# Optimization experiments

Hardware: AMD Instinct MI355X
Metric: run time of the kernel (lower is better)

## Reference

```python
import jax, jax.numpy as jnp
import numpy as np

S, B, N, L, ND = 16, 64, 10000, 128, 1  # seq_len, batch, nodes, latent_dim, node_dim


def setup_inputs() -> dict:
    key = jax.random.key(0)
    ks = jax.random.split(key, 20)
    D_msg = ND + L        # GRU input: [node_feat || time_enc]
    D_h = ND + 2 * L      # attention input: [x || memory || time_enc]
    g = lambda k, shp, s: (jax.random.normal(k, shp, jnp.float32) * s)
    return {
        "x": jax.random.normal(ks[0], (S, B, N, ND), jnp.float32),
        "t": jax.random.uniform(ks[1], (S, B, N, 1), jnp.float32),
        "source": jax.random.randint(ks[2], (S, B, 1), 0, N),
        "target": jax.random.randint(ks[3], (S, B, 1), 0, N),
        "neighbor_mask": jax.random.randint(ks[4], (S, B, N), 0, 2).astype(jnp.bool_),
        # TimeEncoder: cos(t @ w + b)
        "time_w": g(ks[5], (1, L), 1.0),
        "time_b": g(ks[6], (L,), 1.0),
        # MemoryUpdater: GRUCell(input=D_msg, hidden=L)
        "W_ih": g(ks[7], (3 * L, D_msg), 1.0 / np.sqrt(D_msg)),
        "W_hh": g(ks[8], (3 * L, L), 1.0 / np.sqrt(L)),
        "b_ih": jnp.zeros((3 * L,), jnp.float32),
        "b_hh": jnp.zeros((3 * L,), jnp.float32),
        # Attention projections (D_h -> L)
        "Wq": g(ks[9], (D_h, L), 1.0 / np.sqrt(D_h)),
        "bq": jnp.zeros((L,), jnp.float32),
        "Wk": g(ks[10], (D_h, L), 1.0 / np.sqrt(D_h)),
        "bk": jnp.zeros((L,), jnp.float32),
        "Wv": g(ks[11], (D_h, L), 1.0 / np.sqrt(D_h)),
        "bv": jnp.zeros((L,), jnp.float32),
        # final Linear(L -> 1)
        "W_out": g(ks[12], (L, 1), 1.0 / np.sqrt(L)),
        "b_out": jnp.zeros((1,), jnp.float32),
    }


def reference(x, t, source, target, neighbor_mask, time_w, time_b,
              W_ih, W_hh, b_ih, b_hh, Wq, bq, Wk, bk, Wv, bv, W_out, b_out):
    s_len, bsz, n_nodes, _ = x.shape
    lat = time_w.shape[1]
    scale = 1.0 / jnp.sqrt(jnp.float32(lat))
    bidx = jnp.arange(bsz)

    def time_enc(tt):  # [..., 1] -> [..., L]
        return jnp.cos(tt @ time_w + time_b)

    def gru(msg, h):  # torch GRUCell semantics
        gi = msg @ W_ih.T + b_ih
        gh = h @ W_hh.T + b_hh
        i_r, i_z, i_n = jnp.split(gi, 3, axis=-1)
        h_r, h_z, h_n = jnp.split(gh, 3, axis=-1)
        r = jax.nn.sigmoid(i_r + h_r)
        z = jax.nn.sigmoid(i_z + h_z)
        n = jnp.tanh(i_n + r * h_n)
        return (1.0 - z) * n + z * h

    def step(memory, batch):
        xb, tb, src, tgt, mask = batch
        src = src[:, 0]
        tgt = tgt[:, 0]
        dt = time_enc(tb)  # [B, N, L]
        # 1. update memory at source and target nodes
        msg_s = jnp.concatenate([xb[bidx, src], dt[bidx, src]], axis=-1)  # [B, ND+L]
        msg_t = jnp.concatenate([xb[bidx, tgt], dt[bidx, tgt]], axis=-1)
        new_s = gru(msg_s, memory[src])
        new_t = gru(msg_t, memory[tgt])
        mem = memory.at[src].set(new_s).at[tgt].set(new_t)
        # 2. embedding: target query
        tvec = jnp.concatenate([xb[bidx, tgt], mem[tgt]], axis=-1)  # [B, ND+L]
        enc0 = jnp.broadcast_to(jnp.cos(time_b), (bsz, lat))  # time_enc(t=0)
        target_h = jnp.concatenate([tvec, enc0], axis=-1)  # [B, ND+2L]
        # per-node keys/values
        h = jnp.concatenate(
            [xb, jnp.broadcast_to(mem, (bsz, n_nodes, lat)), dt], axis=-1)  # [B, N, ND+2L]
        q = target_h @ Wq + bq          # [B, L]
        k = h @ Wk + bk                 # [B, N, L]
        v = h @ Wv + bv                 # [B, N, L]
        scores = jnp.einsum("bl,bnl->bn", q, k) * scale
        scores = jnp.where(mask, scores, jnp.float32(-1e9))
        attn = jax.nn.softmax(scores, axis=-1)
        z = jnp.einsum("bn,bnl->bl", attn, v)
        logit = z @ W_out + b_out       # [B, 1]
        return mem, logit

    mem0 = jnp.zeros((n_nodes, lat), jnp.float32)
    _, logits = jax.lax.scan(step, mem0, (x, t, source, target, neighbor_mask))
    return logits  # [S, B, 1]
```

## Files before the change

### kernel.cpp

```cpp
#include <hip/hip_runtime.h>
#include <math.h>

#define S_LEN 16
#define BSZ   64
#define NN    10000
#define LAT   128
#define DH    257
#define KTAB  1024
#define CSTRIDE (KTAB + 8)
#define FSTRIDE (KTAB + 4)
#define NTILE 64
#define NTILES 157
#define STEP_BLKS 350
#define SCALE 0.08838834764831845f
#define NEG1E9 -1000000000.0f

struct KP {
    const float *x, *t;
    const int *source, *target;
    const void *maskp;
    const float *tw, *tb_;
    const float *W_ih, *W_hh, *b_ih, *b_hh;
    const float *Wq, *bq, *Wk, *bk, *Wv, *bv, *W_out, *b_out;
    float *out;
    float *mem;
    float *newh[2], *uT[2], *u0qbk[2], *ftab[2], *partials[2];
    float *gtab, *costab;
    float *wv_out, *vconst, *W_ihT, *W_hhT, *BT, *uc, *kw0, *abk, *scal;
    int *modep;
};

__device__ void gru_a_block(const KP& p, float* sm, int r, int snext, int sprev, int zeroH) {
    int tid = threadIdx.x;
    int par = snext & 1;
    float* msg = sm;
    float* h   = sm + 132;
    float* gi3 = sm + 260;
    float* gh3 = sm + 644;
    float* hn  = sm + 1028;
    int*   itab = (int*)(sm + 1156);
    float* axv = sm + 1284;
    unsigned long long* amask = (unsigned long long*)(sm + 1288);
    float* udt = sm + 1296;
    float* red2 = sm + 1424;
    float* fpart = sm + 1440;

    int b = r & 63;
    int idx = (r < 64) ? p.source[snext * BSZ + b] : p.target[snext * BSZ + b];
    if (sprev >= 0 && tid < 128)
        itab[tid] = (tid < 64) ? p.source[sprev * BSZ + tid] : p.target[sprev * BSZ + (tid - 64)];
    const float* xs = p.x + (size_t)(snext * BSZ + b) * NN;
    const float* ts = p.t + (size_t)(snext * BSZ + b) * NN;
    if (tid == 0) msg[0] = xs[idx];
    if (tid < 128) {
        float tv = ts[idx];
        msg[1 + tid] = __cosf(tv * p.tw[tid] + p.tb_[tid]);
    }
    __syncthreads();
    int w = -1;
    if (sprev >= 0) {
        for (int k = 127; k >= 0; --k) if (itab[k] == idx) { w = k; break; }
    }
    if (tid < 128) {
        h[tid] = zeroH ? 0.f
               : (w >= 0 ? p.newh[par ^ 1][w * LAT + tid] : p.mem[(size_t)idx * LAT + tid]);
    }
    __syncthreads();
    if (tid < 128) {
        int j = tid;
        float a0 = p.b_ih[j], a1 = p.b_ih[128 + j], a2 = p.b_ih[256 + j];
#pragma unroll 4
        for (int d = 0; d < 129; ++d) {
            float m = msg[d];
            const float* col = p.W_ihT + d * 384;
            a0 += m * col[j]; a1 += m * col[128 + j]; a2 += m * col[256 + j];
        }
        gi3[j] = a0; gi3[128 + j] = a1; gi3[256 + j] = a2;
    } else {
        int j = tid - 128;
        float a0 = p.b_hh[j], a1 = p.b_hh[128 + j], a2 = p.b_hh[256 + j];
#pragma unroll 4
        for (int l = 0; l < 128; ++l) {
            float hv = h[l];
            const float* col = p.W_hhT + l * 384;
            a0 += hv * col[j]; a1 += hv * col[128 + j]; a2 += hv * col[256 + j];
        }
        gh3[j] = a0; gh3[128 + j] = a1; gh3[256 + j] = a2;
    }
    __syncthreads();
    if (tid < 128) {
        int j = tid;
        float rr = 1.f / (1.f + __expf(-(gi3[j] + gh3[j])));
        float zz = 1.f / (1.f + __expf(-(gi3[128 + j] + gh3[128 + j])));
        float nn2 = tanhf(gi3[256 + j] + rr * gh3[256 + j]);
        float val = (1.f - zz) * nn2 + zz * h[j];
        hn[j] = val;
        p.newh[par][r * LAT + j] = val;
    }
    if (r < 64) return;

    int rT = r - 64;
    int* tg = itab;
    __syncthreads();
    if (tid < 64) tg[tid] = p.target[snext * BSZ + tid];
    __syncthreads();
    unsigned long long mask = 0;
    if (tid < 64) {
        int myt = tg[tid]; int sl = 0;
        for (int k = 0; k < 64; ++k) if (tg[k] == myt) sl = k;
        mask = __ballot(sl == rT);
    }
    if (tid == 0) *amask = mask;
    __syncthreads();
    unsigned long long bl = *amask;
    float* u0qb = p.u0qbk[par];
    float* uTb  = p.uT[par];
    float* ftb  = p.ftab[par];
    while (bl) {
        int b2 = __ffsll((long long)bl) - 1; bl &= bl - 1;
        if (tid == 0) *axv = p.x[(size_t)(snext * BSZ + b2) * NN + tg[b2]];
        __syncthreads();
        float xv = *axv;
        {
            int d = tid;
            float a0 = 0.f, a1 = 0.f;
#pragma unroll 4
            for (int l = 0; l < 128; l += 2) {
                a0 += hn[l] * p.BT[l * 260 + d];
                a1 += hn[l + 1] * p.BT[(l + 1) * 260 + d];
            }
            float a = p.uc[d] + xv * p.kw0[d] + a0 + a1;
            if (d == 0) u0qb[b2] = a;
            else if (d <= 128) uTb[(d - 1) * BSZ + b2] = a;
            else udt[d - 129] = a;
            if (tid == 0) {
                float c0 = 0.f, c1 = 0.f;
#pragma unroll 4
                for (int l = 0; l < 128; l += 2) {
                    c0 += hn[l] * p.BT[l * 260 + 256];
                    c1 += hn[l + 1] * p.BT[(l + 1) * 260 + 256];
                }
                udt[127] = p.uc[256] + xv * p.kw0[256] + c0 + c1;
            }
        }
        if (tid >= 192) {
            int i = tid - 192;
            float a = hn[i] * p.abk[i] + hn[64 + i] * p.abk[64 + i];
            for (int off = 32; off; off >>= 1) a += __shfl_down(a, off, 64);
            if (i == 0) u0qb[64 + b2] = p.scal[0] + xv * p.scal[1] + a;
        }
        __syncthreads();
        {
            int pi = tid & 127, lc = tid >> 7;
            int l0 = lc * 64;
            float a0x = 0.f, a0y = 0.f, a0z = 0.f, a0w = 0.f;
            float a1x = 0.f, a1y = 0.f, a1z = 0.f, a1w = 0.f;
#pragma unroll 4
            for (int l = l0; l < l0 + 64; ++l) {
                float ul = udt[l];
                const float* cp = &p.costab[l * CSTRIDE + pi * 8];
                float4 c0 = *(const float4*)cp;
                float4 c1 = *(const float4*)(cp + 4);
                a0x += ul * c0.x; a0y += ul * c0.y; a0z += ul * c0.z; a0w += ul * c0.w;
                a1x += ul * c1.x; a1y += ul * c1.y; a1z += ul * c1.z; a1w += ul * c1.w;
            }
            if (lc) {
                float* fp = &fpart[pi * 8];
                *(float4*)fp = make_float4(a0x, a0y, a0z, a0w);
                *(float4*)(fp + 4) = make_float4(a1x, a1y, a1z, a1w);
            }
            if (pi == 127) {
                float a = 0.f;
                for (int l = l0; l < l0 + 64; ++l) a += udt[l] * p.costab[l * CSTRIDE + KTAB];
                red2[lc] = a;
            }
            __syncthreads();
            if (lc == 0) {
                const float* fp = &fpart[pi * 8];
                a0x += fp[0]; a0y += fp[1]; a0z += fp[2]; a0w += fp[3];
                a1x += fp[4]; a1y += fp[5]; a1z += fp[6]; a1w += fp[7];
                float* fo = &ftb[b2 * FSTRIDE + pi * 8];
                *(float4*)fo = make_float4(a0x, a0y, a0z, a0w);
                *(float4*)(fo + 4) = make_float4(a1x, a1y, a1z, a1w);
            }
            if (tid == 0) ftb[b2 * FSTRIDE + KTAB] = red2[0] + red2[1];
        }
        __syncthreads();
    }
}

__device__ void combine256(const float* __restrict__ partials, const float* __restrict__ vconst,
                           float* __restrict__ out, float* sm, int b, int ps) {
    int tid = threadIdx.x;
    float m = -3.0e38f, d = 0.f, n = 0.f;
    if (tid < NTILES) {
        float4 v = *((const float4*)partials + b * NTILES + tid);
        m = v.x; d = v.y; n = v.z;
    }
#pragma unroll
    for (int off = 32; off; off >>= 1) {
        float mo = __shfl_down(m, off, 64);
        float d2 = __shfl_down(d, off, 64);
        float n2 = __shfl_down(n, off, 64);
        float M = fmaxf(m, mo);
        float e1 = __expf(m - M), e2 = __expf(mo - M);
        d = d * e1 + d2 * e2; n = n * e1 + n2 * e2; m = M;
    }
    float* red = sm;
    int w = tid >> 6;
    if ((tid & 63) == 0) { red[w * 3] = m; red[w * 3 + 1] = d; red[w * 3 + 2] = n; }
    __syncthreads();
    if (tid == 0) {
        float M = red[0], D = red[1], Nm = red[2];
        for (int k2 = 1; k2 < 4; ++k2) {
            float m2 = red[k2 * 3], d2 = red[k2 * 3 + 1], n2 = red[k2 * 3 + 2];
            float M2 = fmaxf(M, m2);
            float e1 = __expf(M - M2), e2 = __expf(m2 - M2);
            D = D * e1 + d2 * e2; Nm = Nm * e1 + n2 * e2; M = M2;
        }
        out[ps * BSZ + b] = Nm / D + vconst[0];
    }
}

__global__ __launch_bounds__(256) void setup_kernel(KP p) {
    int blk = blockIdx.x, tid = threadIdx.x;
    __shared__ float sm[256];
    if (blk < 256) {
        int gtid = blk * 256 + tid;
        const int GS = 256 * 256;
        for (int i = gtid; i < 129 * 384; i += GS) { int d = i / 384, j = i % 384; p.W_ihT[i] = p.W_ih[j * 129 + d]; }
        for (int i = gtid; i < 128 * 384; i += GS) { int l = i / 384, j = i % 384; p.W_hhT[i] = p.W_hh[j * 128 + l]; }
        for (int pp = gtid; pp <= KTAB; pp += GS) {
            float tv = (float)pp * (1.0f / KTAB);
            for (int l = 0; l < 128; ++l) p.costab[l * CSTRIDE + pp] = __cosf(tv * p.tw[l] + p.tb_[l]);
        }
    } else if (blk == 256) {
        for (int d = tid; d < DH; d += 256) {
            float a = 0.f;
            for (int j = 0; j < LAT; ++j) a += p.Wv[d * LAT + j] * p.W_out[j];
            p.wv_out[d] = a;
        }
        if (tid == 0) {
            float a = p.b_out[0];
            for (int j = 0; j < LAT; ++j) a += p.bv[j] * p.W_out[j];
            p.vconst[0] = a;
        }
        __shared__ int hasHigh, hasFloat;
        if (tid == 0) { hasHigh = 0; hasFloat = 0; }
        __syncthreads();
        const int* mask = (const int*)p.maskp;
        for (int i = tid; i < 4096; i += 256) {
            int v = mask[i];
            if ((unsigned)v > 1u) atomicOr(&hasHigh, 1);
            if (v == 0x3F800000) atomicOr(&hasFloat, 1);
        }
        __syncthreads();
        if (tid == 0) p.modep[0] = hasFloat ? 2 : (hasHigh ? 1 : 0);
    } else if (blk < 385) {
        int l = blk - 257;
        float* vrow = sm;
        if (tid < 128) vrow[tid] = p.Wq[(1 + l) * LAT + tid];
        __syncthreads();
        for (int d = tid; d < DH; d += 256) {
            const float* wkr = p.Wk + d * LAT;
            float a = 0.f;
#pragma unroll 4
            for (int j = 0; j < 128; ++j) a += wkr[j] * vrow[j];
            p.BT[l * 260 + d] = a;
        }
    } else if (blk == 385) {
        float* vrow = sm;
        if (tid < 128) vrow[tid] = p.Wq[tid];
        __syncthreads();
        for (int d = tid; d < DH; d += 256) {
            const float* wkr = p.Wk + d * LAT;
            float a = 0.f;
#pragma unroll 4
            for (int j = 0; j < 128; ++j) a += wkr[j] * vrow[j];
            p.kw0[d] = a;
        }
    } else if (blk == 386) {
        __shared__ float cosv[128], qc[128];
        if (tid < 128) cosv[tid] = __cosf(p.tb_[tid]);
        __syncthreads();
        if (tid < 128) {
            float a = p.bq[tid];
            for (int j = 0; j < 128; ++j) a += cosv[j] * p.Wq[(129 + j) * LAT + tid];
            qc[tid] = a;
        }
        __syncthreads();
        for (int d = tid; d < DH; d += 256) {
            const float* wkr = p.Wk + d * LAT;
            float a = 0.f;
#pragma unroll 4
            for (int j = 0; j < 128; ++j) a += wkr[j] * qc[j];
            p.uc[d] = a;
        }
    } else {
        __shared__ float bkv[128], cosv[128], tpart[128];
        if (tid < 128) { bkv[tid] = p.bk[tid]; cosv[tid] = __cosf(p.tb_[tid]); }
        __syncthreads();
        if (tid < 128) {
            const float* wqr = p.Wq + (1 + tid) * LAT;
            float a = 0.f;
#pragma unroll 4
            for (int j = 0; j < 128; ++j) a += wqr[j] * bkv[j];
            p.abk[tid] = a;
        } else {
            int j = tid - 128;
            const float* wqr = p.Wq + (129 + j) * LAT;
            float a = 0.f;
#pragma unroll 4
            for (int l = 0; l < 128; ++l) a += wqr[l] * bkv[l];
            tpart[j] = cosv[j] * a;
        }
        __syncthreads();
        if (tid == 0) {
            float s0 = 0.f, s1 = 0.f;
            for (int l = 0; l < 128; ++l) { s0 += p.bq[l] * bkv[l]; s1 += p.Wq[l] * bkv[l]; }
            for (int j = 0; j < 128; ++j) s0 += tpart[j];
            p.scal[0] = s0; p.scal[1] = s1;
        }
    }
}

__global__ __launch_bounds__(256) void pre2_kernel(KP p) {
    __shared__ __align__(16) float sm[2464];
    int blk = blockIdx.x, tid = threadIdx.x;
    if (blk < 5) {
        __shared__ float wv_s[LAT];
        if (tid < LAT) wv_s[tid] = p.wv_out[129 + tid];
        __syncthreads();
        int pp = blk * 256 + tid;
        if (pp <= KTAB) {
            float a = 0.f;
            for (int l = 0; l < 128; ++l) a += wv_s[l] * p.costab[l * CSTRIDE + pp];
            p.gtab[pp] = a;
        }
        return;
    }
    gru_a_block(p, sm, blk - 5, 0, -1, 1);
}

__global__ __launch_bounds__(256) void step_kernel(KP p, int s) {
    __shared__ __align__(16) float sm[9472];
    int blk = blockIdx.x, tid = threadIdx.x;
    int par = s & 1;

    if (blk >= 157 && blk < 285) {
        if (s < S_LEN - 1)
            gru_a_block(p, sm, blk - 157, s + 1, s, 0);
        return;
    }
    if (blk == 285) {
        int* idxs  = (int*)sm;
        int* alive = idxs + 128;
        if (tid < 128) idxs[tid] = (tid < 64) ? p.source[s * BSZ + tid] : p.target[s * BSZ + (tid - 64)];
        __syncthreads();
        if (tid < 128) {
            int i2 = idxs[tid];
            int a = 1;
            for (int r2 = tid + 1; r2 < 128; ++r2)
                if (idxs[r2] == i2) { a = 0; break; }
            alive[tid] = a;
        }
        __syncthreads();
        int row = tid >> 1, q2 = tid & 1;
        if (alive[row]) {
            const float4* srcp = (const float4*)(p.newh[par] + row * LAT + q2 * 64);
            float4* dstp = (float4*)(p.mem + (size_t)idxs[row] * LAT + q2 * 64);
#pragma unroll
            for (int j = 0; j < 16; ++j) dstp[j] = srcp[j];
        }
        return;
    }
    if (blk >= 286) {
        if (s > 0) combine256(p.partials[par ^ 1], p.vconst, p.out, sm, blk - 286, s - 1);
        return;
    }

    float* memT   = sm;
    float* uTs    = sm + 4608;
    float* memv_s = sm + 8960;
    float* wv_s   = sm + 9024;
    float* u0_s   = sm + 9152;
    float* qbk_s  = sm + 9216;
    int*   idxs   = (int*)(sm + 9280);
    int*   prow   = idxs + 128;
    int tile = blk;
    int n0 = tile * NTILE;
    int tb = tid >> 4, tn = tid & 15;
    int nvalid = NN - n0; if (nvalid > NTILE) nvalid = NTILE;

    if (tid < 128) wv_s[tid] = p.wv_out[1 + tid];
    if (tid < 64) {
        u0_s[tid] = p.u0qbk[par][tid];
        qbk_s[tid] = p.u0qbk[par][64 + tid];
        memv_s[tid] = 0.f;
    }
    if (tid < 128) idxs[tid] = (tid < 64) ? p.source[s * BSZ + tid] : p.target[s * BSZ + (tid - 64)];
    __syncthreads();
    if (tid < 64) {
        int node = n0 + tid; int w = -1;
        for (int k = 127; k >= 0; --k) if (idxs[k] == node) { w = k; break; }
        prow[tid] = w;
    }

    float acc[4][4];
#pragma unroll
    for (int i = 0; i < 4; ++i)
#pragma unroll
        for (int j = 0; j < 4; ++j) acc[i][j] = 0.f;

    const float* nh = p.newh[par];
    for (int l0 = 0; l0 < 128; l0 += 64) {
        __syncthreads();
        {
            int n_l = tid & 63, lq = (tid >> 6) * 16;
            if (n_l < nvalid) {
                int w = prow[n_l];
                const float* mrow = (w >= 0) ? (nh + w * LAT + l0 + lq)
                                             : (p.mem + (size_t)(n0 + n_l) * LAT + l0 + lq);
                float4 a0 = *(const float4*)(mrow + 0);
                float4 a1 = *(const float4*)(mrow + 4);
                float4 a2 = *(const float4*)(mrow + 8);
                float4 a3 = *(const float4*)(mrow + 12);
                memT[(lq + 0) * 72 + n_l] = a0.x; memT[(lq + 1) * 72 + n_l] = a0.y;
                memT[(lq + 2) * 72 + n_l] = a0.z; memT[(lq + 3) * 72 + n_l] = a0.w;
                memT[(lq + 4) * 72 + n_l] = a1.x; memT[(lq + 5) * 72 + n_l] = a1.y;
                memT[(lq + 6) * 72 + n_l] = a1.z; memT[(lq + 7) * 72 + n_l] = a1.w;
                memT[(lq + 8) * 72 + n_l] = a2.x; memT[(lq + 9) * 72 + n_l] = a2.y;
                memT[(lq + 10) * 72 + n_l] = a2.z; memT[(lq + 11) * 72 + n_l] = a2.w;
                memT[(lq + 12) * 72 + n_l] = a3.x; memT[(lq + 13) * 72 + n_l] = a3.y;
                memT[(lq + 14) * 72 + n_l] = a3.z; memT[(lq + 15) * 72 + n_l] = a3.w;
            } else {
                for (int j = 0; j < 16; ++j) memT[(lq + j) * 72 + n_l] = 0.f;
            }
        }
        {
            int bq4 = (tid & 15) * 4;
            int ll = (tid >> 4) * 4;
            const float* uTb = p.uT[par];
            for (int j = 0; j < 4; ++j) {
                float4 v = *(const float4*)&uTb[(l0 + ll + j) * BSZ + bq4];
                *(float4*)&uTs[(ll + j) * 68 + bq4] = v;
            }
        }
        __syncthreads();
        if (tid < 64) {
            float a = memv_s[tid];
            for (int l = 0; l < 64; ++l) a += wv_s[l0 + l] * memT[l * 72 + tid];
            memv_s[tid] = a;
        }
        for (int l = 0; l < 64; ++l) {
            float4 uv = *(const float4*)&uTs[l * 68 + tb * 4];
            float4 mv = *(const float4*)&memT[l * 72 + tn * 4];
            acc[0][0] += uv.x * mv.x; acc[0][1] += uv.x * mv.y; acc[0][2] += uv.x * mv.z; acc[0][3] += uv.x * mv.w;
            acc[1][0] += uv.y * mv.x; acc[1][1] += uv.y * mv.y; acc[1][2] += uv.y * mv.z; acc[1][3] += uv.y * mv.w;
            acc[2][0] += uv.z * mv.x; acc[2][1] += uv.z * mv.y; acc[2][2] += uv.z * mv.z; acc[2][3] += uv.z * mv.w;
            acc[3][0] += uv.w * mv.x; acc[3][1] += uv.w * mv.y; acc[3][2] += uv.w * mv.z; acc[3][3] += uv.w * mv.w;
        }
    }
    __syncthreads();

    const float c0 = p.wv_out[0];
    int mode = p.modep[0];
    const int* m32 = (const int*)p.maskp;
    const unsigned char* m8 = (const unsigned char*)p.maskp;
    const float* mf = (const float*)p.maskp;
    const float* gtab = p.gtab;
    const float* ftb = p.ftab[par];

    float pm[4], pd[4], pn[4];
#pragma unroll
    for (int i = 0; i < 4; ++i) { pm[i] = -3.0e38f; pd[i] = 0.f; pn[i] = 0.f; }

    for (int i = 0; i < 4; ++i) {
        int b = tb * 4 + i;
        size_t base = (size_t)(s * BSZ + b) * NN + n0 + tn * 4;
        float xv4[4], tv4[4]; int msk[4], vld[4];
        if (tn * 4 + 3 < nvalid) {
            float4 xx = *(const float4*)(p.x + base);
            float4 tt = *(const float4*)(p.t + base);
            xv4[0] = xx.x; xv4[1] = xx.y; xv4[2] = xx.z; xv4[3] = xx.w;
            tv4[0] = tt.x; tv4[1] = tt.y; tv4[2] = tt.z; tv4[3] = tt.w;
            if (mode == 1) {
                unsigned mw = *(const unsigned*)(m8 + base);
                msk[0] = mw & 0xff; msk[1] = (mw >> 8) & 0xff; msk[2] = (mw >> 16) & 0xff; msk[3] = (mw >> 24) & 0xff;
            } else if (mode == 2) {
                float4 mm = *(const float4*)(mf + base);
                msk[0] = (mm.x != 0.f); msk[1] = (mm.y != 0.f); msk[2] = (mm.z != 0.f); msk[3] = (mm.w != 0.f);
            } else {
                int4 mm = *(const int4*)(m32 + base);
                msk[0] = mm.x; msk[1] = mm.y; msk[2] = mm.z; msk[3] = mm.w;
            }
            vld[0] = vld[1] = vld[2] = vld[3] = 1;
        } else {
            for (int j = 0; j < 4; ++j) {
                int n = tn * 4 + j;
                vld[j] = (n < nvalid);
                if (vld[j]) {
                    xv4[j] = p.x[base + j]; tv4[j] = p.t[base + j];
                    msk[j] = (mode == 1) ? (int)m8[base + j] : (mode == 2) ? (mf[base + j] != 0.f) : m32[base + j];
                } else { xv4[j] = 0.f; tv4[j] = 0.f; msk[j] = 0; }
            }
        }
        const float* ft = ftb + b * FSTRIDE;
#pragma unroll
        for (int j = 0; j < 4; ++j) {
            if (!vld[j]) continue;
            float xv = xv4[j], tv = tv4[j];
            float pq = tv * (float)KTAB;
            pq = fminf(fmaxf(pq, 0.f), (float)KTAB - 0.001f);
            int ii = (int)pq;
            float fr = pq - (float)ii;
            float f0 = ft[ii];
            float fv = f0 + (ft[ii + 1] - f0) * fr;
            float g0 = gtab[ii];
            float gv = g0 + (gtab[ii + 1] - g0) * fr;
            float sc = SCALE * (xv * u0_s[b] + acc[i][j] + fv + qbk_s[b]);
            if (msk[j] == 0) sc = NEG1E9;
            float val = xv * c0 + memv_s[tn * 4 + j] + gv;
            if (sc > pm[i]) {
                float a = __expf(pm[i] - sc);
                pd[i] = pd[i] * a + 1.f;
                pn[i] = pn[i] * a + val;
                pm[i] = sc;
            } else {
                float e = __expf(sc - pm[i]);
                pd[i] += e;
                pn[i] += e * val;
            }
        }
    }
#pragma unroll
    for (int mk2 = 1; mk2 < 16; mk2 <<= 1) {
#pragma unroll
        for (int i = 0; i < 4; ++i) {
            float mo = __shfl_xor(pm[i], mk2);
            float d2 = __shfl_xor(pd[i], mk2);
            float n2 = __shfl_xor(pn[i], mk2);
            float M = fmaxf(pm[i], mo);
            float e1 = __expf(pm[i] - M), e2 = __expf(mo - M);
            pd[i] = pd[i] * e1 + d2 * e2;
            pn[i] = pn[i] * e1 + n2 * e2;
            pm[i] = M;
        }
    }
    if (tn == 0) {
#pragma unroll
        for (int i = 0; i < 4; ++i) {
            int b = tb * 4 + i;
            *(float4*)&p.partials[par][(size_t)(b * NTILES + tile) * 4] = make_float4(pm[i], pd[i], pn[i], 0.f);
        }
    }
}

__global__ __launch_bounds__(256) void tail2_kernel(KP p) {
    __shared__ float sm[16];
    combine256(p.partials[(S_LEN - 1) & 1], p.vconst, p.out, sm, blockIdx.x, S_LEN - 1);
}

extern "C" void kernel_launch(void* const* d_in, const int* in_sizes, int n_in,
                              void* d_out, int out_size, void* d_ws, size_t ws_size,
                              hipStream_t stream) {
    KP kp;
    kp.x      = (const float*)d_in[0];
    kp.t      = (const float*)d_in[1];
    kp.source = (const int*)d_in[2];
    kp.target = (const int*)d_in[3];
    kp.maskp  = (const void*)d_in[4];
    kp.tw     = (const float*)d_in[5];
    kp.tb_    = (const float*)d_in[6];
    kp.W_ih   = (const float*)d_in[7];
    kp.W_hh   = (const float*)d_in[8];
    kp.b_ih   = (const float*)d_in[9];
    kp.b_hh   = (const float*)d_in[10];
    kp.Wq     = (const float*)d_in[11];
    kp.bq     = (const float*)d_in[12];
    kp.Wk     = (const float*)d_in[13];
    kp.bk     = (const float*)d_in[14];
    kp.Wv     = (const float*)d_in[15];
    kp.bv     = (const float*)d_in[16];
    kp.W_out  = (const float*)d_in[17];
    kp.b_out  = (const float*)d_in[18];
    kp.out    = (float*)d_out;

    float* w = (float*)d_ws;
    kp.mem        = w; w += (size_t)NN * LAT;
    kp.newh[0]    = w; w += 128 * LAT;
    kp.newh[1]    = w; w += 128 * LAT;
    kp.uT[0]      = w; w += LAT * BSZ;
    kp.uT[1]      = w; w += LAT * BSZ;
    kp.u0qbk[0]   = w; w += 128;
    kp.u0qbk[1]   = w; w += 128;
    kp.ftab[0]    = w; w += BSZ * FSTRIDE;
    kp.ftab[1]    = w; w += BSZ * FSTRIDE;
    kp.partials[0] = w; w += (size_t)BSZ * NTILES * 4;
    kp.partials[1] = w; w += (size_t)BSZ * NTILES * 4;
    kp.gtab       = w; w += 1056;
    kp.costab     = w; w += LAT * CSTRIDE;
    kp.wv_out     = w; w += 288;
    kp.vconst     = w; w += 32;
    kp.W_ihT      = w; w += 129 * 384;
    kp.W_hhT      = w; w += 128 * 384;
    kp.BT         = w; w += 128 * 260;
    kp.uc         = w; w += 288;
    kp.kw0        = w; w += 288;
    kp.abk        = w; w += 128;
    kp.scal       = w; w += 32;
    kp.modep      = (int*)w; w += 32;

    hipMemsetAsync(kp.mem, 0, (size_t)NN * LAT * sizeof(float), stream);
    setup_kernel<<<388, 256, 0, stream>>>(kp);
    pre2_kernel<<<133, 256, 0, stream>>>(kp);
    for (int s = 0; s < S_LEN; ++s)
        step_kernel<<<STEP_BLKS, 256, 0, stream>>>(kp, s);
    tail2_kernel<<<64, 256, 0, stream>>>(kp);
}
```

Measured before the change: 832.2 us.

## Split attention tiles across batch quarters and prefetch per-node inputs early

Each attention block now handles 16 batch rows of a 64-node tile instead of all 64, so the grid grows from 157 to 628 attention blocks. Each thread keeps one batch row with four accumulators rather than a 4x4 register tile. The x, t and mask loads and the f/g table gathers are issued before the memory-tile GEMM so their latency overlaps it. The price is that every node tile is reloaded and transposed four times, and each block does less arithmetic per load.

```diff
diff --git a/kernel.cpp b/kernel.cpp
--- a/kernel.cpp
+++ b/kernel.cpp
@@ -11,7 +11,12 @@
 #define FSTRIDE (KTAB + 4)
 #define NTILE 64
 #define NTILES 157
-#define STEP_BLKS 350
+#define BSPLIT 4
+#define ATTN_BLKS (NTILES * BSPLIT)
+#define GRU0 ATTN_BLKS
+#define SCAT (ATTN_BLKS + 128)
+#define COMB0 (SCAT + 1)
+#define STEP_BLKS (COMB0 + 64)
 #define SCALE 0.08838834764831845f
 #define NEG1E9 -1000000000.0f
 
@@ -343,16 +348,16 @@
 }
 
 __global__ __launch_bounds__(256) void step_kernel(KP p, int s) {
-    __shared__ __align__(16) float sm[9472];
+    __shared__ __align__(16) float sm[7680];
     int blk = blockIdx.x, tid = threadIdx.x;
     int par = s & 1;
 
-    if (blk >= 157 && blk < 285) {
+    if (blk >= GRU0 && blk < SCAT) {
         if (s < S_LEN - 1)
-            gru_a_block(p, sm, blk - 157, s + 1, s, 0);
+            gru_a_block(p, sm, blk - GRU0, s + 1, s, 0);
         return;
     }
-    if (blk == 285) {
+    if (blk == SCAT) {
         int* idxs  = (int*)sm;
         int* alive = idxs + 128;
         if (tid < 128) idxs[tid] = (tid < 64) ? p.source[s * BSZ + tid] : p.target[s * BSZ + (tid - 64)];
@@ -374,30 +379,82 @@
         }
         return;
     }
-    if (blk >= 286) {
-        if (s > 0) combine256(p.partials[par ^ 1], p.vconst, p.out, sm, blk - 286, s - 1);
+    if (blk >= COMB0) {
+        if (s > 0) combine256(p.partials[par ^ 1], p.vconst, p.out, sm, blk - COMB0, s - 1);
         return;
     }
 
     float* memT   = sm;
     float* uTs    = sm + 4608;
-    float* memv_s = sm + 8960;
-    float* wv_s   = sm + 9024;
-    float* u0_s   = sm + 9152;
-    float* qbk_s  = sm + 9216;
-    int*   idxs   = (int*)(sm + 9280);
-    int*   prow   = idxs + 128;
-    int tile = blk;
-    int n0 = tile * NTILE;
+    float* wv_s   = sm + 7168;
+    float* memv_s = sm + 7296;
+    float* u0_s   = sm + 7360;
+    float* qbk_s  = sm + 7376;
+    int*   idxs   = (int*)(sm + 7392);
+    int*   prow   = (int*)(sm + 7520);
+
+    int tile = blk >> 2, bq = blk & 3;
+    int n0 = tile * NTILE, b0 = bq * 16;
     int tb = tid >> 4, tn = tid & 15;
+    int b = b0 + tb;
     int nvalid = NN - n0; if (nvalid > NTILE) nvalid = NTILE;
 
+    int mode = p.modep[0];
+    const int* m32 = (const int*)p.maskp;
+    const unsigned char* m8 = (const unsigned char*)p.maskp;
+    const float* mf = (const float*)p.maskp;
+    size_t base = (size_t)(s * BSZ + b) * NN + n0 + tn * 4;
+    float xv4[4], tv4[4]; int msk[4], vld[4];
+    if (tn * 4 + 3 < nvalid) {
+        float4 xx = *(const float4*)(p.x + base);
+        float4 tt = *(const float4*)(p.t + base);
+        xv4[0] = xx.x; xv4[1] = xx.y; xv4[2] = xx.z; xv4[3] = xx.w;
+        tv4[0] = tt.x; tv4[1] = tt.y; tv4[2] = tt.z; tv4[3] = tt.w;
+        if (mode == 1) {
+            unsigned mw = *(const unsigned*)(m8 + base);
+            msk[0] = mw & 0xff; msk[1] = (mw >> 8) & 0xff; msk[2] = (mw >> 16) & 0xff; msk[3] = (mw >> 24) & 0xff;
+        } else if (mode == 2) {
+            float4 mm = *(const float4*)(mf + base);
+            msk[0] = (mm.x != 0.f); msk[1] = (mm.y != 0.f); msk[2] = (mm.z != 0.f); msk[3] = (mm.w != 0.f);
+        } else {
+            int4 mm = *(const int4*)(m32 + base);
+            msk[0] = mm.x; msk[1] = mm.y; msk[2] = mm.z; msk[3] = mm.w;
+        }
+        vld[0] = vld[1] = vld[2] = vld[3] = 1;
+    } else {
+        for (int j = 0; j < 4; ++j) {
+            int n = tn * 4 + j;
+            vld[j] = (n < nvalid);
+            if (vld[j]) {
+                xv4[j] = p.x[base + j]; tv4[j] = p.t[base + j];
+                msk[j] = (mode == 1) ? (int)m8[base + j] : (mode == 2) ? (mf[base + j] != 0.f) : m32[base + j];
+            } else { xv4[j] = 0.f; tv4[j] = 0.f; msk[j] = 0; }
+        }
+    }
+    const float* ft = p.ftab[par] + b * FSTRIDE;
+    const float* gtab = p.gtab;
+    float fr[4], f0v[4], f1v[4], g0v[4], g1v[4];
+#pragma unroll
+    for (int j = 0; j < 4; ++j) {
+        float pq = tv4[j] * (float)KTAB;
+        pq = fminf(fmaxf(pq, 0.f), (float)KTAB - 0.001f);
+        int ii = (int)pq;
+        fr[j] = pq - (float)ii;
+        f0v[j] = ft[ii]; f1v[j] = ft[ii + 1];
+        g0v[j] = gtab[ii]; g1v[j] = gtab[ii + 1];
+    }
+
+    {
+        int l = tid >> 1, bb = (tid & 1) * 8;
+        const float* uTb = p.uT[par];
+        float4 v0 = *(const float4*)&uTb[l * BSZ + b0 + bb];
+        float4 v1 = *(const float4*)&uTb[l * BSZ + b0 + bb + 4];
+        *(float4*)&uTs[l * 20 + bb] = v0;
+        *(float4*)&uTs[l * 20 + bb + 4] = v1;
+    }
     if (tid < 128) wv_s[tid] = p.wv_out[1 + tid];
-    if (tid < 64) {
-        u0_s[tid] = p.u0qbk[par][tid];
-        qbk_s[tid] = p.u0qbk[par][64 + tid];
-        memv_s[tid] = 0.f;
-    }
+    if (tid < 16) { u0_s[tid] = p.u0qbk[par][b0 + tid]; qbk_s[tid] = p.u0qbk[par][64 + b0 + tid]; }
+    if (tid < 64) memv_s[tid] = 0.f;
     if (tid < 128) idxs[tid] = (tid < 64) ? p.source[s * BSZ + tid] : p.target[s * BSZ + (tid - 64)];
     __syncthreads();
     if (tid < 64) {
@@ -406,12 +463,7 @@
         prow[tid] = w;
     }
 
-    float acc[4][4];
-#pragma unroll
-    for (int i = 0; i < 4; ++i)
-#pragma unroll
-        for (int j = 0; j < 4; ++j) acc[i][j] = 0.f;
-
+    float acc0 = 0.f, acc1 = 0.f, acc2 = 0.f, acc3 = 0.f;
     const float* nh = p.newh[par];
     for (int l0 = 0; l0 < 128; l0 += 64) {
         __syncthreads();
@@ -437,15 +489,6 @@
                 for (int j = 0; j < 16; ++j) memT[(lq + j) * 72 + n_l] = 0.f;
             }
         }
-        {
-            int bq4 = (tid & 15) * 4;
-            int ll = (tid >> 4) * 4;
-            const float* uTb = p.uT[par];
-            for (int j = 0; j < 4; ++j) {
-                float4 v = *(const float4*)&uTb[(l0 + ll + j) * BSZ + bq4];
-                *(float4*)&uTs[(ll + j) * 68 + bq4] = v;
-            }
-        }
         __syncthreads();
         if (tid < 64) {
             float a = memv_s[tid];
@@ -453,107 +496,48 @@
             memv_s[tid] = a;
         }
         for (int l = 0; l < 64; ++l) {
-            float4 uv = *(const float4*)&uTs[l * 68 + tb * 4];
+            float u = uTs[(l0 + l) * 20 + tb];
             float4 mv = *(const float4*)&memT[l * 72 + tn * 4];
-            acc[0][0] += uv.x * mv.x; acc[0][1] += uv.x * mv.y; acc[0][2] += uv.x * mv.z; acc[0][3] += uv.x * mv.w;
-            acc[1][0] += uv.y * mv.x; acc[1][1] += uv.y * mv.y; acc[1][2] += uv.y * mv.z; acc[1][3] += uv.y * mv.w;
-            acc[2][0] += uv.z * mv.x; acc[2][1] += uv.z * mv.y; acc[2][2] += uv.z * mv.z; acc[2][3] += uv.z * mv.w;
-            acc[3][0] += uv.w * mv.x; acc[3][1] += uv.w * mv.y; acc[3][2] += uv.w * mv.z; acc[3][3] += uv.w * mv.w;
+            acc0 += u * mv.x; acc1 += u * mv.y; acc2 += u * mv.z; acc3 += u * mv.w;
         }
     }
     __syncthreads();
 
     const float c0 = p.wv_out[0];
-    int mode = p.modep[0];
-    const int* m32 = (const int*)p.maskp;
-    const unsigned char* m8 = (const unsigned char*)p.maskp;
-    const float* mf = (const float*)p.maskp;
-    const float* gtab = p.gtab;
-    const float* ftb = p.ftab[par];
-
-    float pm[4], pd[4], pn[4];
+    float accs[4] = {acc0, acc1, acc2, acc3};
+    float pm = -3.0e38f, pd = 0.f, pn = 0.f;
 #pragma unroll
-    for (int i = 0; i < 4; ++i) { pm[i] = -3.0e38f; pd[i] = 0.f; pn[i] = 0.f; }
-
-    for (int i = 0; i < 4; ++i) {
-        int b = tb * 4 + i;
-        size_t base = (size_t)(s * BSZ + b) * NN + n0 + tn * 4;
-        float xv4[4], tv4[4]; int msk[4], vld[4];
-        if (tn * 4 + 3 < nvalid) {
-            float4 xx = *(const float4*)(p.x + base);
-            float4 tt = *(const float4*)(p.t + base);
-            xv4[0] = xx.x; xv4[1] = xx.y; xv4[2] = xx.z; xv4[3] = xx.w;
-            tv4[0] = tt.x; tv4[1] = tt.y; tv4[2] = tt.z; tv4[3] = tt.w;
-            if (mode == 1) {
-                unsigned mw = *(const unsigned*)(m8 + base);
-                msk[0] = mw & 0xff; msk[1] = (mw >> 8) & 0xff; msk[2] = (mw >> 16) & 0xff; msk[3] = (mw >> 24) & 0xff;
-            } else if (mode == 2) {
-                float4 mm = *(const float4*)(mf + base);
-                msk[0] = (mm.x != 0.f); msk[1] = (mm.y != 0.f); msk[2] = (mm.z != 0.f); msk[3] = (mm.w != 0.f);
-            } else {
-                int4 mm = *(const int4*)(m32 + base);
-                msk[0] = mm.x; msk[1] = mm.y; msk[2] = mm.z; msk[3] = mm.w;
-            }
-            vld[0] = vld[1] = vld[2] = vld[3] = 1;
+    for (int j = 0; j < 4; ++j) {
+        if (!vld[j]) continue;
+        float fv = f0v[j] + (f1v[j] - f0v[j]) * fr[j];
+        float gv = g0v[j] + (g1v[j] - g0v[j]) * fr[j];
+        float sc = SCALE * (xv4[j] * u0_s[tb] + accs[j] + fv + qbk_s[tb]);
+        if (msk[j] == 0) sc = NEG1E9;
+        float val = xv4[j] * c0 + memv_s[tn * 4 + j] + gv;
+        if (sc > pm) {
+            float a = __expf(pm - sc);
+            pd = pd * a + 1.f;
+            pn = pn * a + val;
+            pm = sc;
         } else {
-            for (int j = 0; j < 4; ++j) {
-                int n = tn * 4 + j;
-                vld[j] = (n < nvalid);
-                if (vld[j]) {
-                    xv4[j] = p.x[base + j]; tv4[j] = p.t[base + j];
-                    msk[j] = (mode == 1) ? (int)m8[base + j] : (mode == 2) ? (mf[base + j] != 0.f) : m32[base + j];
-                } else { xv4[j] = 0.f; tv4[j] = 0.f; msk[j] = 0; }
-            }
-        }
-        const float* ft = ftb + b * FSTRIDE;
-#pragma unroll
-        for (int j = 0; j < 4; ++j) {
-            if (!vld[j]) continue;
-            float xv = xv4[j], tv = tv4[j];
-            float pq = tv * (float)KTAB;
-            pq = fminf(fmaxf(pq, 0.f), (float)KTAB - 0.001f);
-            int ii = (int)pq;
-            float fr = pq - (float)ii;
-            float f0 = ft[ii];
-            float fv = f0 + (ft[ii + 1] - f0) * fr;
-            float g0 = gtab[ii];
-            float gv = g0 + (gtab[ii + 1] - g0) * fr;
-            float sc = SCALE * (xv * u0_s[b] + acc[i][j] + fv + qbk_s[b]);
-            if (msk[j] == 0) sc = NEG1E9;
-            float val = xv * c0 + memv_s[tn * 4 + j] + gv;
-            if (sc > pm[i]) {
-                float a = __expf(pm[i] - sc);
-                pd[i] = pd[i] * a + 1.f;
-                pn[i] = pn[i] * a + val;
-                pm[i] = sc;
-            } else {
-                float e = __expf(sc - pm[i]);
-                pd[i] += e;
-                pn[i] += e * val;
-            }
+            float e = __expf(sc - pm);
+            pd += e;
+            pn += e * val;
         }
     }
 #pragma unroll
     for (int mk2 = 1; mk2 < 16; mk2 <<= 1) {
-#pragma unroll
-        for (int i = 0; i < 4; ++i) {
-            float mo = __shfl_xor(pm[i], mk2);
-            float d2 = __shfl_xor(pd[i], mk2);
-            float n2 = __shfl_xor(pn[i], mk2);
-            float M = fmaxf(pm[i], mo);
-            float e1 = __expf(pm[i] - M), e2 = __expf(mo - M);
-            pd[i] = pd[i] * e1 + d2 * e2;
-            pn[i] = pn[i] * e1 + n2 * e2;
-            pm[i] = M;
-        }
-    }
-    if (tn == 0) {
-#pragma unroll
-        for (int i = 0; i < 4; ++i) {
-            int b = tb * 4 + i;
-            *(float4*)&p.partials[par][(size_t)(b * NTILES + tile) * 4] = make_float4(pm[i], pd[i], pn[i], 0.f);
-        }
-    }
+        float mo = __shfl_xor(pm, mk2);
+        float d2 = __shfl_xor(pd, mk2);
+        float n2 = __shfl_xor(pn, mk2);
+        float M = fmaxf(pm, mo);
+        float e1 = __expf(pm - M), e2 = __expf(mo - M);
+        pd = pd * e1 + d2 * e2;
+        pn = pn * e1 + n2 * e2;
+        pm = M;
+    }
+    if (tn == 0)
+        *(float4*)&p.partials[par][(size_t)(b * NTILES + tile) * 4] = make_float4(pm, pd, pn, 0.f);
 }
 
 __global__ __launch_bounds__(256) void tail2_kernel(KP p) {
```

Result: slower. 1.894 ms (+127.6%).
